# Performance work log

Hardware: AMD Instinct MI355X
Metric: run time of the kernel (lower is better)

Reference implementation:

```python
import jax, jax.numpy as jnp
import numpy as np

N_NODES = 50000


def gcn_layer(x, W, b, src, dst, n_nodes):
    # PyG GCNConv(normalize=True): add self-loops, deg^-1/2 sym norm,
    # x' = D^-1/2 (A+I) D^-1/2 (x W) + b, aggregation at dst (col).
    h = x @ W  # [N, out]
    ones = jnp.ones(src.shape[0], dtype=h.dtype)
    deg = jax.ops.segment_sum(ones, dst, num_segments=n_nodes) + 1.0  # +1 self-loop
    dinv = jax.lax.rsqrt(deg)  # [N]
    norm = dinv[src] * dinv[dst]  # per-edge coefficient
    msg = h[src] * norm[:, None]  # [E, out] gather
    agg = jax.ops.segment_sum(msg, dst, num_segments=n_nodes)  # scatter-add
    agg = agg + h * (dinv * dinv)[:, None]  # self-loop term (norm = dinv_i^2)
    return agg + b


def setup_inputs() -> dict:
    key = jax.random.key(0)
    k1, k2, k3, k4, k5 = jax.random.split(key, 5)
    x = jax.random.normal(k1, (N_NODES, 96), dtype=jnp.float32)
    edge_index = jax.random.randint(k2, (2, 800000), 0, N_NODES, dtype=jnp.int64)
    # Glorot-ish weights, zero bias (PyG default init style)
    W1 = jax.random.normal(k3, (96, 96), dtype=jnp.float32) * (1.0 / np.sqrt(96))
    b1 = jnp.zeros((96,), dtype=jnp.float32)
    W2 = jax.random.normal(k4, (96, 64), dtype=jnp.float32) * (1.0 / np.sqrt(96))
    b2 = jnp.zeros((64,), dtype=jnp.float32)
    return {"x": x, "edge_index": edge_index, "W1": W1, "b1": b1, "W2": W2, "b2": b2}


def reference(x, edge_index, W1, b1, W2, b2):
    src, dst = edge_index[0], edge_index[1]
    n = x.shape[0]
    h = gcn_layer(x, W1, b1, src, dst, n)
    out = gcn_layer(h, W2, b2, src, dst, n)
    return out
```

## Files before the change

kernel.cpp:

```cpp
#include <hip/hip_runtime.h>

#define N_NODES 50000
#define N_EDGES 800000
#define NBLKA 200
#define EPB (N_EDGES / NBLKA)
#define NBUCK 196
#define MSCAN (256 * NBLKA)
#define GEMMBLKS ((N_NODES + 63) / 64)

typedef unsigned int uint;
typedef unsigned short ushort;

__device__ __forceinline__ uint bf16pack(float a, float b) {
    uint ua = __float_as_uint(a); ua = (ua + 0x7FFFu + ((ua >> 16) & 1u)) >> 16;
    uint ub = __float_as_uint(b); ub = (ub + 0x7FFFu + ((ub >> 16) & 1u)) >> 16;
    return ua | (ub << 16);
}
#define BF_LO(U) __uint_as_float((U) << 16)
#define BF_HI(U) __uint_as_float((U) & 0xFFFF0000u)

__global__ void histA_kernel(const int* __restrict__ dst, int* __restrict__ hist) {
    __shared__ int h[256];
    h[threadIdx.x] = 0;
    __syncthreads();
    const int4* d4 = (const int4*)(dst + blockIdx.x * EPB);
    for (int i = threadIdx.x; i < EPB / 4; i += 256) {
        int4 v = d4[i];
        atomicAdd(&h[v.x >> 8], 1);
        atomicAdd(&h[v.y >> 8], 1);
        atomicAdd(&h[v.z >> 8], 1);
        atomicAdd(&h[v.w >> 8], 1);
    }
    __syncthreads();
    hist[threadIdx.x * NBLKA + blockIdx.x] = h[threadIdx.x];
}

__global__ void scan1_kernel(const int* __restrict__ in, int* __restrict__ out,
                             int* __restrict__ bsum, int n) {
    __shared__ int s[256];
    int i = blockIdx.x * 256 + threadIdx.x;
    int v = (i < n) ? in[i] : 0;
    s[threadIdx.x] = v;
    __syncthreads();
    for (int d = 1; d < 256; d <<= 1) {
        int t = (threadIdx.x >= d) ? s[threadIdx.x - d] : 0;
        __syncthreads();
        s[threadIdx.x] += t;
        __syncthreads();
    }
    if (i < n) out[i] = s[threadIdx.x] - v;
    if (threadIdx.x == 255) bsum[blockIdx.x] = s[255];
}

__global__ void scan2_wfuse_kernel(int* __restrict__ bsum, int* __restrict__ boff, int nb,
                                   const float* __restrict__ W1, const float* __restrict__ W2,
                                   const float* __restrict__ b1, float* __restrict__ W12,
                                   float* __restrict__ bw) {
    if (blockIdx.x == 0) {
        __shared__ int s[256];
        int t = threadIdx.x;
        int v = (t < nb) ? bsum[t] : 0;
        s[t] = v;
        __syncthreads();
        for (int d = 1; d < 256; d <<= 1) {
            int x = (t >= d) ? s[t - d] : 0;
            __syncthreads();
            s[t] += x;
            __syncthreads();
        }
        if (t < nb) boff[t] = s[t] - v;
        if (t == nb - 1) boff[nb] = s[t];
    } else {
        int idx = (blockIdx.x - 1) * 256 + threadIdx.x;
        if (idx < 96 * 64) {
            int k = idx >> 6, nn = idx & 63;
            float s = 0.0f;
#pragma unroll
            for (int j = 0; j < 96; ++j) s = fmaf(W1[k * 96 + j], W2[j * 64 + nn], s);
            W12[idx] = s;
        } else if (idx < 96 * 64 + 64) {
            int nn = idx - 96 * 64;
            float s = 0.0f;
#pragma unroll
            for (int j = 0; j < 96; ++j) s = fmaf(b1[j], W2[j * 64 + nn], s);
            bw[nn] = s;
        }
    }
}

#define FMA4(ACC, SCL, WV)                                                     \
    ACC.x = fmaf(SCL, WV.x, ACC.x);                                            \
    ACC.y = fmaf(SCL, WV.y, ACC.y);                                            \
    ACC.z = fmaf(SCL, WV.z, ACC.z);                                            \
    ACC.w = fmaf(SCL, WV.w, ACC.w);

__global__ __launch_bounds__(256)
void scatter_gemm_kernel(const int* __restrict__ src, const int* __restrict__ dst,
                         const int* __restrict__ scanned, const int* __restrict__ boff,
                         uint* __restrict__ ebuf,
                         const float* __restrict__ A, const float* __restrict__ W,
                         ushort* __restrict__ y16, int M) {
    __shared__ float smem[64 * 100];
    int tid = threadIdx.x;

    if (blockIdx.x < NBLKA) {
        int* off = (int*)smem;
        int gi = tid * NBLKA + blockIdx.x;
        off[tid] = scanned[gi] + boff[gi >> 8];
        __syncthreads();
        int base = blockIdx.x * EPB;
        for (int i = base + tid; i < base + EPB; i += 256) {
            int s = src[i];
            int d = dst[i];
            int p = atomicAdd(&off[d >> 8], 1);
            ebuf[p] = (uint)s | ((uint)(d & 255) << 16);
        }
        return;
    }

    int bid = blockIdx.x - NBLKA;
    float* sA = smem;
    long row0 = (long)bid * 64;
    {
        const float4* A4 = (const float4*)A;
        long base4 = row0 * 24;
        long lim = (long)M * 24 - 1;
        for (int f = tid; f < 64 * 24; f += 256) {
            long g = base4 + f;
            if (g > lim) g = lim;
            float4 v = A4[g];
            int r = f / 24, kc = f - r * 24;
            *(float4*)(sA + r * 100 + kc * 4) = v;
        }
    }
    __syncthreads();

    int tx = tid & 15;
    int ty = tid >> 4;
    float4 acc0 = {0, 0, 0, 0};
    float4 acc1 = {0, 0, 0, 0};
    float4 acc2 = {0, 0, 0, 0};
    float4 acc3 = {0, 0, 0, 0};
    const float* pa = sA + ty * 4 * 100;
    const float4* W4 = (const float4*)W;

#pragma unroll 1
    for (int k = 0; k < 96; k += 4) {
        float4 a0 = *(const float4*)(pa + 0 * 100 + k);
        float4 a1 = *(const float4*)(pa + 1 * 100 + k);
        float4 a2 = *(const float4*)(pa + 2 * 100 + k);
        float4 a3 = *(const float4*)(pa + 3 * 100 + k);
        float4 w0 = W4[(k + 0) * 16 + tx];
        float4 w1 = W4[(k + 1) * 16 + tx];
        float4 w2 = W4[(k + 2) * 16 + tx];
        float4 w3 = W4[(k + 3) * 16 + tx];
        FMA4(acc0, a0.x, w0) FMA4(acc0, a0.y, w1) FMA4(acc0, a0.z, w2) FMA4(acc0, a0.w, w3)
        FMA4(acc1, a1.x, w0) FMA4(acc1, a1.y, w1) FMA4(acc1, a1.z, w2) FMA4(acc1, a1.w, w3)
        FMA4(acc2, a2.x, w0) FMA4(acc2, a2.y, w1) FMA4(acc2, a2.z, w2) FMA4(acc2, a2.w, w3)
        FMA4(acc3, a3.x, w0) FMA4(acc3, a3.y, w1) FMA4(acc3, a3.z, w2) FMA4(acc3, a3.w, w3)
    }

    long r0 = row0 + ty * 4;
    uint2 p0 = {bf16pack(acc0.x, acc0.y), bf16pack(acc0.z, acc0.w)};
    uint2 p1 = {bf16pack(acc1.x, acc1.y), bf16pack(acc1.z, acc1.w)};
    uint2 p2 = {bf16pack(acc2.x, acc2.y), bf16pack(acc2.z, acc2.w)};
    uint2 p3 = {bf16pack(acc3.x, acc3.y), bf16pack(acc3.z, acc3.w)};
    if (r0 + 0 < M) *(uint2*)(y16 + (r0 + 0) * 64 + tx * 4) = p0;
    if (r0 + 1 < M) *(uint2*)(y16 + (r0 + 1) * 64 + tx * 4) = p1;
    if (r0 + 2 < M) *(uint2*)(y16 + (r0 + 2) * 64 + tx * 4) = p2;
    if (r0 + 3 < M) *(uint2*)(y16 + (r0 + 3) * 64 + tx * 4) = p3;
}

__global__ void bucket_kernel(const uint* __restrict__ ebuf, const int* __restrict__ scanned,
                              const int* __restrict__ boff, int* __restrict__ rowstart,
                              float* __restrict__ dinv, ushort* __restrict__ esrc) {
    __shared__ int cnt[256];
    __shared__ int cur[256];
    __shared__ int s[256];
    int k = blockIdx.x;
    int tid = threadIdx.x;
    int i0 = k * NBLKA, i1 = (k + 1) * NBLKA;
    int base = scanned[i0] + boff[i0 >> 8];
    int end  = (k == NBUCK - 1) ? N_EDGES : (scanned[i1] + boff[i1 >> 8]);
    cnt[tid] = 0;
    __syncthreads();
    for (int i = base + tid; i < end; i += 256)
        atomicAdd(&cnt[(ebuf[i] >> 16) & 255], 1);
    __syncthreads();
    int v = cnt[tid];
    s[tid] = v;
    __syncthreads();
    for (int d = 1; d < 256; d <<= 1) {
        int t = (tid >= d) ? s[tid - d] : 0;
        __syncthreads();
        s[tid] += t;
        __syncthreads();
    }
    int excl = s[tid] - v;
    int node = (k << 8) + tid;
    cur[tid] = base + excl;
    if (node < N_NODES) {
        rowstart[node] = base + excl;
        dinv[node] = rsqrtf((float)v + 1.0f);
    }
    if (k == 0 && tid == 0) rowstart[N_NODES] = N_EDGES;
    __syncthreads();
    for (int i = base + tid; i < end; i += 256) {
        uint e = ebuf[i];
        int p = atomicAdd(&cur[(e >> 16) & 255], 1);
        esrc[p] = (ushort)(e & 0xFFFFu);
    }
}

#define DECFMA(A0, A1, A2, A3, A4, A5, A6, A7, C, V)                           \
    A0 = fmaf(BF_LO(V.x), C, A0); A1 = fmaf(BF_HI(V.x), C, A1);                \
    A2 = fmaf(BF_LO(V.y), C, A2); A3 = fmaf(BF_HI(V.y), C, A3);                \
    A4 = fmaf(BF_LO(V.z), C, A4); A5 = fmaf(BF_HI(V.z), C, A5);                \
    A6 = fmaf(BF_LO(V.w), C, A6); A7 = fmaf(BF_HI(V.w), C, A7);

template <bool FINAL>
__global__ __launch_bounds__(256)
void agg_kernel(const ushort* __restrict__ yin, const int* __restrict__ rowstart,
                const ushort* __restrict__ esrc, const float* __restrict__ dinv,
                const float* __restrict__ bw, const float* __restrict__ b2,
                ushort* __restrict__ zout, float* __restrict__ fout, int n) {
    int gid = (blockIdx.x * blockDim.x + threadIdx.x) >> 4;
    int gl = threadIdx.x & 15;
    if (gid >= n) return;
    int rs = rowstart[gid];
    int re = rowstart[gid + 1];
    float di = dinv[gid];
    int sub = gl >> 3;
    int q = gl & 7;
    int wbase = (threadIdx.x & 63) & 48;
    const uint4* yrow = (const uint4*)yin;
    float P0 = 0, P1 = 0, P2 = 0, P3 = 0, P4 = 0, P5 = 0, P6 = 0, P7 = 0;
    float sd = 0.0f;

    for (int base = rs; base < re; base += 16) {
        int idx = base + gl;
        bool ok = idx < re;
        int sj = ok ? (int)esrc[idx] : 0;
        float dj = ok ? dinv[sj] : 0.0f;
        sd += dj;
        int nn = re - base;
        if (nn > 16) nn = 16;
        for (int it = 0; it * 2 < nn; ++it) {
            int e = it * 2 + sub;
            int sl = wbase + e;
            int s0 = __shfl(sj, sl);
            float c0 = __shfl(dj, sl);
            uint4 v0 = yrow[(long)s0 * 8 + q];
            DECFMA(P0, P1, P2, P3, P4, P5, P6, P7, c0, v0)
        }
    }

    float t0 = P0 + __shfl_xor(P0, 8);
    float t1 = P1 + __shfl_xor(P1, 8);
    float t2 = P2 + __shfl_xor(P2, 8);
    float t3 = P3 + __shfl_xor(P3, 8);
    float t4 = P4 + __shfl_xor(P4, 8);
    float t5 = P5 + __shfl_xor(P5, 8);
    float t6 = P6 + __shfl_xor(P6, 8);
    float t7 = P7 + __shfl_xor(P7, 8);

    uint4 sv = yrow[(long)gid * 8 + q];
    float dii = di * di;
    float o0 = fmaf(t0, di, BF_LO(sv.x) * dii);
    float o1 = fmaf(t1, di, BF_HI(sv.x) * dii);
    float o2 = fmaf(t2, di, BF_LO(sv.y) * dii);
    float o3 = fmaf(t3, di, BF_HI(sv.y) * dii);
    float o4 = fmaf(t4, di, BF_LO(sv.z) * dii);
    float o5 = fmaf(t5, di, BF_HI(sv.z) * dii);
    float o6 = fmaf(t6, di, BF_LO(sv.w) * dii);
    float o7 = fmaf(t7, di, BF_HI(sv.w) * dii);

    if (FINAL) {
        sd += __shfl_xor(sd, 1); sd += __shfl_xor(sd, 2);
        sd += __shfl_xor(sd, 4); sd += __shfl_xor(sd, 8);
        float si = di * (di + sd);
        int fo = q * 8;
        float4 bwa = *(const float4*)(bw + fo);
        float4 bwb = *(const float4*)(bw + fo + 4);
        float4 b2a = *(const float4*)(b2 + fo);
        float4 b2b = *(const float4*)(b2 + fo + 4);
        o0 = fmaf(si, bwa.x, o0) + b2a.x;
        o1 = fmaf(si, bwa.y, o1) + b2a.y;
        o2 = fmaf(si, bwa.z, o2) + b2a.z;
        o3 = fmaf(si, bwa.w, o3) + b2a.w;
        o4 = fmaf(si, bwb.x, o4) + b2b.x;
        o5 = fmaf(si, bwb.y, o5) + b2b.y;
        o6 = fmaf(si, bwb.z, o6) + b2b.z;
        o7 = fmaf(si, bwb.w, o7) + b2b.w;
        if (sub == 0) {
            float4 wa = {o0, o1, o2, o3};
            float4 wb = {o4, o5, o6, o7};
            *(float4*)(fout + (long)gid * 64 + q * 8) = wa;
            *(float4*)(fout + (long)gid * 64 + q * 8 + 4) = wb;
        }
    } else {
        if (sub == 0) {
            uint4 pk;
            pk.x = bf16pack(o0, o1);
            pk.y = bf16pack(o2, o3);
            pk.z = bf16pack(o4, o5);
            pk.w = bf16pack(o6, o7);
            *(uint4*)(zout + (long)gid * 64 + q * 8) = pk;
        }
    }
}

extern "C" void kernel_launch(void* const* d_in, const int* in_sizes, int n_in,
                              void* d_out, int out_size, void* d_ws, size_t ws_size,
                              hipStream_t stream) {
    const float* x  = (const float*)d_in[0];
    const int*   ei = (const int*)d_in[1];
    const float* W1 = (const float*)d_in[2];
    const float* b1 = (const float*)d_in[3];
    const float* W2 = (const float*)d_in[4];
    const float* b2 = (const float*)d_in[5];
    float* out = (float*)d_out;

    const int* src = ei;
    const int* dst = ei + N_EDGES;

    char* ws = (char*)d_ws;
    float*  dinv     = (float*) (ws + 0);
    int*    rowstart = (int*)   (ws + 204800);
    int*    hist     = (int*)   (ws + 409600);
    int*    scanned  = (int*)   (ws + 614400);
    int*    bsum     = (int*)   (ws + 823296);
    int*    boff     = (int*)   (ws + 824320);
    float*  W12      = (float*) (ws + 825344);
    float*  bw       = (float*) (ws + 849920);
    ushort* esrc     = (ushort*)(ws + 850432);
    ushort* y16      = (ushort*)(ws + 2450432);
    uint*   ebuf     = (uint*)  (ws + 8850432);
    ushort* z16      = (ushort*)(ws + 8850432);

    histA_kernel<<<NBLKA, 256, 0, stream>>>(dst, hist);
    scan1_kernel<<<MSCAN / 256, 256, 0, stream>>>(hist, scanned, bsum, MSCAN);
    scan2_wfuse_kernel<<<26, 256, 0, stream>>>(bsum, boff, MSCAN / 256,
                                               W1, W2, b1, W12, bw);
    scatter_gemm_kernel<<<NBLKA + GEMMBLKS, 256, 0, stream>>>(
        src, dst, scanned, boff, ebuf, x, W12, y16, N_NODES);

    bucket_kernel<<<NBUCK, 256, 0, stream>>>(ebuf, scanned, boff, rowstart, dinv, esrc);

    int aggBlocks = (N_NODES * 16 + 255) / 256;
    agg_kernel<false><<<aggBlocks, 256, 0, stream>>>(y16, rowstart, esrc, dinv,
                                                     bw, b2, z16, out, N_NODES);
    agg_kernel<true><<<aggBlocks, 256, 0, stream>>>(z16, rowstart, esrc, dinv,
                                                    bw, b2, z16, out, N_NODES);
}
```

Measured before the change: 86.25 us.

## Replace three-pass bucket scan with per-bin totals and atomic cursor allocation

Folds the W1·W2 precompute into the histogram kernel and replaces the 200-block prefix scan plus its second pass with a single-block scan over per-bucket totals. Scatter blocks then claim their output ranges with an atomicAdd on a per-bucket cursor. This removes one kernel launch and the large scanned-array traffic. In exchange, edge order within a bucket becomes nondeterministic, which can change the floating-point summation order downstream.

Result: slower. 91.56 us (+6.2%).

```diff
diff --git a/kernel.cpp b/kernel.cpp
--- a/kernel.cpp
+++ b/kernel.cpp
@@ -5,7 +5,6 @@
 #define NBLKA 200
 #define EPB (N_EDGES / NBLKA)
 #define NBUCK 196
-#define MSCAN (256 * NBLKA)
 #define GEMMBLKS ((N_NODES + 63) / 64)
 
 typedef unsigned int uint;
@@ -19,59 +18,27 @@
 #define BF_LO(U) __uint_as_float((U) << 16)
 #define BF_HI(U) __uint_as_float((U) & 0xFFFF0000u)
 
-__global__ void histA_kernel(const int* __restrict__ dst, int* __restrict__ hist) {
-    __shared__ int h[256];
-    h[threadIdx.x] = 0;
-    __syncthreads();
-    const int4* d4 = (const int4*)(dst + blockIdx.x * EPB);
-    for (int i = threadIdx.x; i < EPB / 4; i += 256) {
-        int4 v = d4[i];
-        atomicAdd(&h[v.x >> 8], 1);
-        atomicAdd(&h[v.y >> 8], 1);
-        atomicAdd(&h[v.z >> 8], 1);
-        atomicAdd(&h[v.w >> 8], 1);
-    }
-    __syncthreads();
-    hist[threadIdx.x * NBLKA + blockIdx.x] = h[threadIdx.x];
-}
-
-__global__ void scan1_kernel(const int* __restrict__ in, int* __restrict__ out,
-                             int* __restrict__ bsum, int n) {
-    __shared__ int s[256];
-    int i = blockIdx.x * 256 + threadIdx.x;
-    int v = (i < n) ? in[i] : 0;
-    s[threadIdx.x] = v;
-    __syncthreads();
-    for (int d = 1; d < 256; d <<= 1) {
-        int t = (threadIdx.x >= d) ? s[threadIdx.x - d] : 0;
-        __syncthreads();
-        s[threadIdx.x] += t;
-        __syncthreads();
-    }
-    if (i < n) out[i] = s[threadIdx.x] - v;
-    if (threadIdx.x == 255) bsum[blockIdx.x] = s[255];
-}
-
-__global__ void scan2_wfuse_kernel(int* __restrict__ bsum, int* __restrict__ boff, int nb,
+__global__ void histA_wfuse_kernel(const int* __restrict__ dst,
+                                   int* __restrict__ blockcounts,
                                    const float* __restrict__ W1, const float* __restrict__ W2,
                                    const float* __restrict__ b1, float* __restrict__ W12,
                                    float* __restrict__ bw) {
-    if (blockIdx.x == 0) {
-        __shared__ int s[256];
-        int t = threadIdx.x;
-        int v = (t < nb) ? bsum[t] : 0;
-        s[t] = v;
-        __syncthreads();
-        for (int d = 1; d < 256; d <<= 1) {
-            int x = (t >= d) ? s[t - d] : 0;
-            __syncthreads();
-            s[t] += x;
-            __syncthreads();
-        }
-        if (t < nb) boff[t] = s[t] - v;
-        if (t == nb - 1) boff[nb] = s[t];
+    if (blockIdx.x < NBLKA) {
+        __shared__ int h[256];
+        h[threadIdx.x] = 0;
+        __syncthreads();
+        const int4* d4 = (const int4*)(dst + blockIdx.x * EPB);
+        for (int i = threadIdx.x; i < EPB / 4; i += 256) {
+            int4 v = d4[i];
+            atomicAdd(&h[v.x >> 8], 1);
+            atomicAdd(&h[v.y >> 8], 1);
+            atomicAdd(&h[v.z >> 8], 1);
+            atomicAdd(&h[v.w >> 8], 1);
+        }
+        __syncthreads();
+        blockcounts[blockIdx.x * 256 + threadIdx.x] = h[threadIdx.x];
     } else {
-        int idx = (blockIdx.x - 1) * 256 + threadIdx.x;
+        int idx = (blockIdx.x - NBLKA) * 256 + threadIdx.x;
         if (idx < 96 * 64) {
             int k = idx >> 6, nn = idx & 63;
             float s = 0.0f;
@@ -88,6 +55,26 @@
     }
 }
 
+__global__ void scanbins_kernel(const int* __restrict__ blockcounts,
+                                int* __restrict__ basearr, int* __restrict__ cursor) {
+    __shared__ int s[256];
+    int t = threadIdx.x;
+    int v = 0;
+    for (int b = 0; b < NBLKA; ++b) v += blockcounts[b * 256 + t];
+    s[t] = v;
+    __syncthreads();
+    for (int d = 1; d < 256; d <<= 1) {
+        int x = (t >= d) ? s[t - d] : 0;
+        __syncthreads();
+        s[t] += x;
+        __syncthreads();
+    }
+    int excl = s[t] - v;
+    basearr[t] = excl;
+    cursor[t] = excl;
+    if (t == 255) basearr[256] = s[255];
+}
+
 #define FMA4(ACC, SCL, WV)                                                     \
     ACC.x = fmaf(SCL, WV.x, ACC.x);                                            \
     ACC.y = fmaf(SCL, WV.y, ACC.y);                                            \
@@ -96,7 +83,7 @@
 
 __global__ __launch_bounds__(256)
 void scatter_gemm_kernel(const int* __restrict__ src, const int* __restrict__ dst,
-                         const int* __restrict__ scanned, const int* __restrict__ boff,
+                         const int* __restrict__ blockcounts, int* __restrict__ cursor,
                          uint* __restrict__ ebuf,
                          const float* __restrict__ A, const float* __restrict__ W,
                          ushort* __restrict__ y16, int M) {
@@ -105,8 +92,8 @@
 
     if (blockIdx.x < NBLKA) {
         int* off = (int*)smem;
-        int gi = tid * NBLKA + blockIdx.x;
-        off[tid] = scanned[gi] + boff[gi >> 8];
+        int mc = blockcounts[blockIdx.x * 256 + tid];
+        off[tid] = atomicAdd(&cursor[tid], mc);
         __syncthreads();
         int base = blockIdx.x * EPB;
         for (int i = base + tid; i < base + EPB; i += 256) {
@@ -171,17 +158,16 @@
     if (r0 + 3 < M) *(uint2*)(y16 + (r0 + 3) * 64 + tx * 4) = p3;
 }
 
-__global__ void bucket_kernel(const uint* __restrict__ ebuf, const int* __restrict__ scanned,
-                              const int* __restrict__ boff, int* __restrict__ rowstart,
-                              float* __restrict__ dinv, ushort* __restrict__ esrc) {
+__global__ void bucket_kernel(const uint* __restrict__ ebuf, const int* __restrict__ basearr,
+                              int* __restrict__ rowstart, float* __restrict__ dinv,
+                              ushort* __restrict__ esrc) {
     __shared__ int cnt[256];
     __shared__ int cur[256];
     __shared__ int s[256];
     int k = blockIdx.x;
     int tid = threadIdx.x;
-    int i0 = k * NBLKA, i1 = (k + 1) * NBLKA;
-    int base = scanned[i0] + boff[i0 >> 8];
-    int end  = (k == NBUCK - 1) ? N_EDGES : (scanned[i1] + boff[i1 >> 8]);
+    int base = basearr[k];
+    int end  = basearr[k + 1];
     cnt[tid] = 0;
     __syncthreads();
     for (int i = base + tid; i < end; i += 256)
@@ -325,28 +311,24 @@
     const int* dst = ei + N_EDGES;
 
     char* ws = (char*)d_ws;
-    float*  dinv     = (float*) (ws + 0);
-    int*    rowstart = (int*)   (ws + 204800);
-    int*    hist     = (int*)   (ws + 409600);
-    int*    scanned  = (int*)   (ws + 614400);
-    int*    bsum     = (int*)   (ws + 823296);
-    int*    boff     = (int*)   (ws + 824320);
-    float*  W12      = (float*) (ws + 825344);
-    float*  bw       = (float*) (ws + 849920);
-    ushort* esrc     = (ushort*)(ws + 850432);
-    ushort* y16      = (ushort*)(ws + 2450432);
-    uint*   ebuf     = (uint*)  (ws + 8850432);
-    ushort* z16      = (ushort*)(ws + 8850432);
-
-    histA_kernel<<<NBLKA, 256, 0, stream>>>(dst, hist);
-    scan1_kernel<<<MSCAN / 256, 256, 0, stream>>>(hist, scanned, bsum, MSCAN);
-    scan2_wfuse_kernel<<<26, 256, 0, stream>>>(bsum, boff, MSCAN / 256,
-                                               W1, W2, b1, W12, bw);
+    float*  dinv        = (float*) (ws + 0);
+    int*    rowstart    = (int*)   (ws + 204800);
+    int*    blockcounts = (int*)   (ws + 409600);
+    int*    basearr     = (int*)   (ws + 614400);
+    int*    cursor      = (int*)   (ws + 615936);
+    float*  W12         = (float*) (ws + 616960);
+    float*  bw          = (float*) (ws + 641536);
+    ushort* esrc        = (ushort*)(ws + 642048);
+    ushort* y16         = (ushort*)(ws + 2242048);
+    uint*   ebuf        = (uint*)  (ws + 8642048);
+    ushort* z16         = (ushort*)(ws + 8642048);
+
+    histA_wfuse_kernel<<<NBLKA + 25, 256, 0, stream>>>(dst, blockcounts,
+                                                       W1, W2, b1, W12, bw);
+    scanbins_kernel<<<1, 256, 0, stream>>>(blockcounts, basearr, cursor);
     scatter_gemm_kernel<<<NBLKA + GEMMBLKS, 256, 0, stream>>>(
-        src, dst, scanned, boff, ebuf, x, W12, y16, N_NODES);
-
-    bucket_kernel<<<NBUCK, 256, 0, stream>>>(ebuf, scanned, boff, rowstart, dinv, esrc);
-
+        src, dst, blockcounts, cursor, ebuf, x, W12, y16, N_NODES);
+    bucket_kernel<<<NBUCK, 256, 0, stream>>>(ebuf, basearr, rowstart, dinv, esrc);
     int aggBlocks = (N_NODES * 16 + 255) / 256;
     agg_kernel<false><<<aggBlocks, 256, 0, stream>>>(y16, rowstart, esrc, dinv,
                                                      bw, b2, z16, out, N_NODES);
```
